# Kernel optimization log

Hardware: AMD Instinct MI355X
Metric: run time of the kernel (lower is better)

The kernel has to match this reference:

```python
import jax, jax.numpy as jnp
import numpy as np

NUM_LAYERS = 16
ALPHA = 1.0
EPS = 1e-20

def setup_inputs() -> dict:
    key = jax.random.key(0)
    k1, k2, k3, k4 = jax.random.split(key, 4)
    B, S, M, G = 8, 9, 8, 512
    M2 = M * M
    return {
        "dict_real": jax.random.normal(k1, (B, S, M2, G), dtype=jnp.float32),
        "dict_imag": jax.random.normal(k2, (B, S, M2, G), dtype=jnp.float32),
        "cov_real": jax.random.normal(k3, (B, S, M, M), dtype=jnp.float32),
        "cov_imag": jax.random.normal(k4, (B, S, M, M), dtype=jnp.float32),
    }

def reference(dict_real, dict_imag, cov_real, cov_imag):
    D = (dict_real + 1j * dict_imag).astype(jnp.complex64)   # (B,S,M2,G) dictionary_band
    C = (cov_real + 1j * cov_imag).astype(jnp.complex64)     # (B,S,M,M) covariance matrix
    B, S, M, _ = C.shape
    G = D.shape[-1]
    # covariance_vector = cov.transpose(2,3).reshape(B,S,M2,1)
    r = jnp.swapaxes(C, 2, 3).reshape(B, S, M * M, 1)
    Dh = jnp.conj(jnp.swapaxes(D, 2, 3))                     # (B,S,G,M2)
    DhD = jnp.matmul(Dh, D)                                  # (B,S,G,G) Hermitian PSD
    Dhr = jnp.matmul(Dh, r)                                  # (B,S,G,1)
    # initial spectrum: real part, L2-normalized over grid dim
    res = jnp.real(Dhr).astype(jnp.float32)
    res = res / (jnp.linalg.norm(res, axis=2, keepdims=True) + EPS)
    # gamma = 1 / max|eig(D^H D)|; Hermitian PSD so eigvalsh gives same max magnitude
    eig = jnp.linalg.eigvalsh(DhD)                           # (B,S,G) real
    gamma = 1.0 / jnp.max(jnp.abs(eig), axis=2, keepdims=True)        # (B,S,1)
    lam = 0.5 * jnp.max(jnp.abs(Dhr), axis=2, keepdims=True).reshape(B, S, 1)
    theta = (ALPHA * lam * gamma).reshape(B, S, 1, 1)
    g = gamma.reshape(B, S, 1, 1).astype(jnp.complex64)
    I = jnp.eye(G, dtype=jnp.complex64)
    Wt = I - g * DhD                                         # (B,S,G,G)
    Wer = g * Dhr                                            # We @ r, constant per layer

    def step(res_c, _):
        s = jnp.matmul(Wt, res_c.astype(jnp.complex64)) + Wer
        res_new = jax.nn.relu(jnp.abs(s) - theta)            # soft-shrinkage on magnitude
        return res_new, res_new

    res_final, res_all = jax.lax.scan(step, res, None, length=NUM_LAYERS)
    result_init_all = jnp.moveaxis(res_all, 0, 2)            # (B,S,L,G,1)

    def minmax_norm(x):
        lo = jnp.min(x, axis=2, keepdims=True)
        hi = jnp.max(x, axis=2, keepdims=True)
        return (x - lo) / (hi - lo + EPS)

    result_ave = minmax_norm(jnp.mean(res_final, axis=1, keepdims=True).astype(jnp.float32))
    result = minmax_norm(res_final)
    return (result, result_ave, result_init_all)
```

## Files before the change

### kernel.cpp

```cpp
#include <hip/hip_runtime.h>
#include <math.h>

#define N_SQ   7
#define INV_P  (1.0f / 256.0f)
#define EPS_F  1e-20f
#define PH     72
#define PQ     67

typedef _Float16 h2    __attribute__((ext_vector_type(2)));
typedef _Float16 f16x8 __attribute__((ext_vector_type(8)));
typedef float    f32x4 __attribute__((ext_vector_type(4)));

__device__ inline float cdot2(h2 a, h2 b, float c) {
#if __has_builtin(__builtin_amdgcn_fdot2)
    return __builtin_amdgcn_fdot2(a, b, c, false);
#else
    return c + (float)a.x * (float)b.x + (float)a.y * (float)b.y;
#endif
}
__device__ inline h2 bch2(unsigned int x) { return __builtin_bit_cast(h2, x); }
__device__ inline h2 bch2f(float x)       { return __builtin_bit_cast(h2, x); }
__device__ inline float bcf(h2 x)         { return __builtin_bit_cast(float, x); }


__global__ __launch_bounds__(512, 1) void ista_main_kernel(
    const float* __restrict__ Dre, const float* __restrict__ Dim,
    const float* __restrict__ Cre, const float* __restrict__ Cim,
    float* __restrict__ out, float* __restrict__ ws)
{
    const int bs = blockIdx.x;
    const int t  = threadIdx.x;
    const int wv = t >> 6;
    const int ln = t & 63;
    const int c16 = ln & 15;
    const int qd  = ln >> 4;
    const float* __restrict__ dre = Dre + (size_t)bs * 32768;
    const float* __restrict__ dim = Dim + (size_t)bs * 32768;

    __shared__ __align__(16) float uBuf[9216];
    _Float16* ShRe = (_Float16*)uBuf;
    _Float16* ShIm = (_Float16*)uBuf + 64 * PH;
    float*    Q1   = uBuf + 4608;
    float*    sUp  = uBuf;
    float*    sHu  = uBuf + 1024;
    _Float16* sResH = (_Float16*)(uBuf + 1152);
    __shared__ __align__(16) float s_r[128];
    __shared__ float s_red[16];
    __shared__ float s_scal[8];

    if (t < 64) {
        int i = t >> 3, j = t & 7;
        s_r[2 * t]     = Cre[bs * 64 + j * 8 + i];
        s_r[2 * t + 1] = Cim[bs * 64 + j * 8 + i];
    }
    __syncthreads();

    float dhr_re = 0.f, dhr_im = 0.f;
    h2 dV[64];
    #pragma unroll
    for (int m = 0; m < 64; ++m) {
        float ar = dre[m * 512 + t], ai = dim[m * 512 + t];
        dV[m] = h2{(_Float16)ar, (_Float16)ai};
        float rr = s_r[2 * m], ri = s_r[2 * m + 1];
        dhr_re += ar * rr + ai * ri;
        dhr_im += ar * ri - ai * rr;
    }
    {
        float sv = dhr_re * dhr_re;
        float mv = sqrtf(dhr_re * dhr_re + dhr_im * dhr_im);
        for (int off = 32; off; off >>= 1) {
            sv += __shfl_down(sv, off, 64);
            mv = fmaxf(mv, __shfl_down(mv, off, 64));
        }
        if (ln == 0) { s_red[wv] = sv; s_red[8 + wv] = mv; }
        __syncthreads();
        if (t == 0) {
            float ss = 0.f, mm = 0.f;
            for (int k = 0; k < 8; ++k) { ss += s_red[k]; mm = fmaxf(mm, s_red[8 + k]); }
            s_scal[7] = ss; s_scal[2] = mm;
        }
        __syncthreads();
    }
    float res_g = dhr_re / (sqrtf(s_scal[7]) + EPS_F);

    const int tau0 = 2 * wv, tau1 = 2 * wv + 1;
    const int I0 = tau0 >> 2, J0 = tau0 & 3;
    const int I1 = tau1 >> 2, J1 = tau1 & 3;

    auto epilogue = [&](f32x4 P0, f32x4 Qa0, f32x4 P1, f32x4 Qa1, bool first, bool last) {
        #pragma unroll
        for (int r = 0; r < 4; ++r) {
            Q1[(I0 * 16 + qd * 4 + r) * PQ + J0 * 16 + c16] = Qa0[r];
            Q1[(I1 * 16 + qd * 4 + r) * PQ + J1 * 16 + c16] = Qa1[r];
        }
        float dv = 0.f;
        if (I0 == J0) {
            #pragma unroll
            for (int r = 0; r < 4; ++r) if (qd * 4 + r == c16) dv = fmaxf(dv, fabsf(P0[r]));
        }
        if (I1 == J1) {
            #pragma unroll
            for (int r = 0; r < 4; ++r) if (qd * 4 + r == c16) dv = fmaxf(dv, fabsf(P1[r]));
        }
        for (int off = 32; off; off >>= 1) dv = fmaxf(dv, __shfl_down(dv, off, 64));
        if (ln == 0) s_red[wv] = dv;
        __syncthreads();
        if (t == 0) {
            float m = 0.f;
            for (int k = 0; k < 8; ++k) m = fmaxf(m, s_red[k]);
            s_scal[3] = first ? logf(m) : 2.f * s_scal[3] + logf(m);
            s_scal[4] = 1.f / m;
        }
        __syncthreads();
        float ic = s_scal[4];
        float ci0[4], ci1[4];
        #pragma unroll
        for (int r = 0; r < 4; ++r) {
            ci0[r] = Qa0[r] - Q1[(J0 * 16 + c16) * PQ + I0 * 16 + qd * 4 + r];
            ci1[r] = Qa1[r] - Q1[(J1 * 16 + c16) * PQ + I1 * 16 + qd * 4 + r];
        }
        if (!last) {
            #pragma unroll
            for (int r = 0; r < 4; ++r) {
                ShRe[(I0 * 16 + qd * 4 + r) * PH + J0 * 16 + c16] = (_Float16)(P0[r] * ic);
                ShIm[(I0 * 16 + qd * 4 + r) * PH + J0 * 16 + c16] = (_Float16)(ci0[r] * ic);
                ShRe[(I1 * 16 + qd * 4 + r) * PH + J1 * 16 + c16] = (_Float16)(P1[r] * ic);
                ShIm[(I1 * 16 + qd * 4 + r) * PH + J1 * 16 + c16] = (_Float16)(ci1[r] * ic);
            }
            __syncthreads();
        } else {
            float fr = 0.f;
            #pragma unroll
            for (int r = 0; r < 4; ++r)
                fr += P0[r] * P0[r] + ci0[r] * ci0[r] + P1[r] * P1[r] + ci1[r] * ci1[r];
            fr *= ic * ic;
            for (int off = 32; off; off >>= 1) fr += __shfl_down(fr, off, 64);
            if (ln == 0) s_red[wv] = fr;
            __syncthreads();
            if (t == 0) {
                float fsum = 0.f;
                for (int k = 0; k < 8; ++k) fsum += s_red[k];
                float loglam = (2.f * s_scal[3] + logf(fsum)) * INV_P;
                float gamma = expf(-loglam);
                s_scal[0] = gamma;
                s_scal[1] = 0.5f * s_scal[2] * gamma;
            }
            __syncthreads();
        }
    };

    h2 du_re[32], du_im[32];
    f32x4 gP0 = {0.f, 0.f, 0.f, 0.f}, gQ0 = {0.f, 0.f, 0.f, 0.f};
    f32x4 gP1 = {0.f, 0.f, 0.f, 0.f}, gQ1 = {0.f, 0.f, 0.f, 0.f};
    {
        const int srow = t >> 4;
        const int scb  = (t & 15) * 4;
        float4 pr0, pi0, pr1, pi1;
        pr0 = *(const float4*)&dre[srow * 512 + scb];
        pi0 = *(const float4*)&dim[srow * 512 + scb];
        pr1 = *(const float4*)&dre[(srow + 32) * 512 + scb];
        pi1 = *(const float4*)&dim[(srow + 32) * 512 + scb];
        for (int ch = 0; ch < 8; ++ch) {
            *(h2*)&ShRe[srow * PH + scb]     = h2{(_Float16)pr0.x, (_Float16)pr0.y};
            *(h2*)&ShRe[srow * PH + scb + 2] = h2{(_Float16)pr0.z, (_Float16)pr0.w};
            *(h2*)&ShIm[srow * PH + scb]     = h2{(_Float16)pi0.x, (_Float16)pi0.y};
            *(h2*)&ShIm[srow * PH + scb + 2] = h2{(_Float16)pi0.z, (_Float16)pi0.w};
            *(h2*)&ShRe[(srow + 32) * PH + scb]     = h2{(_Float16)pr1.x, (_Float16)pr1.y};
            *(h2*)&ShRe[(srow + 32) * PH + scb + 2] = h2{(_Float16)pr1.z, (_Float16)pr1.w};
            *(h2*)&ShIm[(srow + 32) * PH + scb]     = h2{(_Float16)pi1.x, (_Float16)pi1.y};
            *(h2*)&ShIm[(srow + 32) * PH + scb + 2] = h2{(_Float16)pi1.z, (_Float16)pi1.w};
            if (ch < 7) {
                int gc = (ch + 1) * 64;
                pr0 = *(const float4*)&dre[srow * 512 + gc + scb];
                pi0 = *(const float4*)&dim[srow * 512 + gc + scb];
                pr1 = *(const float4*)&dre[(srow + 32) * 512 + gc + scb];
                pi1 = *(const float4*)&dim[(srow + 32) * 512 + gc + scb];
            }
            __syncthreads();
            #pragma unroll
            for (int ks = 0; ks < 64; ks += 32) {
                f16x8 arI0 = *(const f16x8*)&ShRe[(I0 * 16 + c16) * PH + ks + qd * 8];
                f16x8 aiI0 = *(const f16x8*)&ShIm[(I0 * 16 + c16) * PH + ks + qd * 8];
                f16x8 arJ0 = *(const f16x8*)&ShRe[(J0 * 16 + c16) * PH + ks + qd * 8];
                f16x8 aiJ0 = *(const f16x8*)&ShIm[(J0 * 16 + c16) * PH + ks + qd * 8];
                gP0 = __builtin_amdgcn_mfma_f32_16x16x32_f16(arI0, arJ0, gP0, 0, 0, 0);
                gP0 = __builtin_amdgcn_mfma_f32_16x16x32_f16(aiI0, aiJ0, gP0, 0, 0, 0);
                gQ0 = __builtin_amdgcn_mfma_f32_16x16x32_f16(aiI0, arJ0, gQ0, 0, 0, 0);
                f16x8 arI1 = *(const f16x8*)&ShRe[(I1 * 16 + c16) * PH + ks + qd * 8];
                f16x8 aiI1 = *(const f16x8*)&ShIm[(I1 * 16 + c16) * PH + ks + qd * 8];
                f16x8 arJ1 = *(const f16x8*)&ShRe[(J1 * 16 + c16) * PH + ks + qd * 8];
                f16x8 aiJ1 = *(const f16x8*)&ShIm[(J1 * 16 + c16) * PH + ks + qd * 8];
                gP1 = __builtin_amdgcn_mfma_f32_16x16x32_f16(arI1, arJ1, gP1, 0, 0, 0);
                gP1 = __builtin_amdgcn_mfma_f32_16x16x32_f16(aiI1, aiJ1, gP1, 0, 0, 0);
                gQ1 = __builtin_amdgcn_mfma_f32_16x16x32_f16(aiI1, arJ1, gQ1, 0, 0, 0);
            }
            if (ch == wv) {
                #pragma unroll
                for (int c = 0; c < 8; ++c) {
                    uint4 aw = *(const uint4*)&ShRe[ln * PH + 8 * c];
                    du_re[4 * c + 0] = bch2(aw.x); du_re[4 * c + 1] = bch2(aw.y);
                    du_re[4 * c + 2] = bch2(aw.z); du_re[4 * c + 3] = bch2(aw.w);
                    uint4 bw = *(const uint4*)&ShIm[ln * PH + 8 * c];
                    du_im[4 * c + 0] = bch2(bw.x); du_im[4 * c + 1] = bch2(bw.y);
                    du_im[4 * c + 2] = bch2(bw.z); du_im[4 * c + 3] = bch2(bw.w);
                }
            }
            __syncthreads();
        }
    }
    epilogue(gP0, gQ0, gP1, gQ1, true, false);

    for (int sq = 0; sq < N_SQ; ++sq) {
        f32x4 P0 = {0.f, 0.f, 0.f, 0.f}, Qa0 = {0.f, 0.f, 0.f, 0.f};
        f32x4 P1 = {0.f, 0.f, 0.f, 0.f}, Qa1 = {0.f, 0.f, 0.f, 0.f};
        #pragma unroll
        for (int ks = 0; ks < 64; ks += 32) {
            f16x8 arI0 = *(const f16x8*)&ShRe[(I0 * 16 + c16) * PH + ks + qd * 8];
            f16x8 aiI0 = *(const f16x8*)&ShIm[(I0 * 16 + c16) * PH + ks + qd * 8];
            f16x8 arJ0 = *(const f16x8*)&ShRe[(J0 * 16 + c16) * PH + ks + qd * 8];
            f16x8 aiJ0 = *(const f16x8*)&ShIm[(J0 * 16 + c16) * PH + ks + qd * 8];
            P0  = __builtin_amdgcn_mfma_f32_16x16x32_f16(arI0, arJ0, P0, 0, 0, 0);
            P0  = __builtin_amdgcn_mfma_f32_16x16x32_f16(aiI0, aiJ0, P0, 0, 0, 0);
            Qa0 = __builtin_amdgcn_mfma_f32_16x16x32_f16(aiI0, arJ0, Qa0, 0, 0, 0);
            f16x8 arI1 = *(const f16x8*)&ShRe[(I1 * 16 + c16) * PH + ks + qd * 8];
            f16x8 aiI1 = *(const f16x8*)&ShIm[(I1 * 16 + c16) * PH + ks + qd * 8];
            f16x8 arJ1 = *(const f16x8*)&ShRe[(J1 * 16 + c16) * PH + ks + qd * 8];
            f16x8 aiJ1 = *(const f16x8*)&ShIm[(J1 * 16 + c16) * PH + ks + qd * 8];
            P1  = __builtin_amdgcn_mfma_f32_16x16x32_f16(arI1, arJ1, P1, 0, 0, 0);
            P1  = __builtin_amdgcn_mfma_f32_16x16x32_f16(aiI1, aiJ1, P1, 0, 0, 0);
            Qa1 = __builtin_amdgcn_mfma_f32_16x16x32_f16(aiI1, arJ1, Qa1, 0, 0, 0);
        }
        epilogue(P0, Qa0, P1, Qa1, false, sq == N_SQ - 1);
    }

    const float gamma = s_scal[0];
    const float theta = s_scal[1];
    float* out_init = out + 40960 + (size_t)bs * 8192;
    const int resh_base = 64 * wv;

    for (int l = 0; l < 16; ++l) {
        sResH[t] = (_Float16)res_g;
        float upR = 0.f, upI = 0.f;
        #pragma unroll
        for (int c = 0; c < 8; ++c) {
            uint4 rw = *(const uint4*)&sResH[resh_base + 8 * c];
            h2 r0 = bch2(rw.x), r1 = bch2(rw.y), r2 = bch2(rw.z), r3 = bch2(rw.w);
            upR = cdot2(du_re[4 * c + 0], r0, upR);  upI = cdot2(du_im[4 * c + 0], r0, upI);
            upR = cdot2(du_re[4 * c + 1], r1, upR);  upI = cdot2(du_im[4 * c + 1], r1, upI);
            upR = cdot2(du_re[4 * c + 2], r2, upR);  upI = cdot2(du_im[4 * c + 2], r2, upI);
            upR = cdot2(du_re[4 * c + 3], r3, upR);  upI = cdot2(du_im[4 * c + 3], r3, upI);
        }
        *(float2*)&sUp[(wv * 64 + ln) * 2] = make_float2(upR, upI);
        __syncthreads();
        if (wv == 0) {
            float ufR = 0.f, ufI = 0.f;
            #pragma unroll
            for (int w8 = 0; w8 < 8; ++w8) {
                float2 p = *(const float2*)&sUp[(w8 * 64 + ln) * 2];
                ufR += p.x; ufI += p.y;
            }
            h2 hu1 = h2{(_Float16)ufR, (_Float16)ufI};
            h2 hu2 = h2{(_Float16)ufI, (_Float16)(-ufR)};
            *(float2*)&sHu[2 * ln] = make_float2(bcf(hu1), bcf(hu2));
        }
        __syncthreads();
        float wR = 0.f, wI = 0.f;
        #pragma unroll
        for (int mm = 0; mm < 32; ++mm) {
            float4 hq = *(const float4*)&sHu[4 * mm];
            wR = cdot2(dV[2 * mm],     bch2f(hq.x), wR);
            wI = cdot2(dV[2 * mm],     bch2f(hq.y), wI);
            wR = cdot2(dV[2 * mm + 1], bch2f(hq.z), wR);
            wI = cdot2(dV[2 * mm + 1], bch2f(hq.w), wI);
        }
        float sre = res_g + gamma * (dhr_re - wR);
        float sim = gamma * (dhr_im - wI);
        float mag = sqrtf(sre * sre + sim * sim);
        res_g = fmaxf(mag - theta, 0.f);
        out_init[l * 512 + t] = res_g;
    }

    {
        float mn = res_g, mx = res_g;
        for (int off = 32; off; off >>= 1) {
            mn = fminf(mn, __shfl_down(mn, off, 64));
            mx = fmaxf(mx, __shfl_down(mx, off, 64));
        }
        if (ln == 0) { s_red[wv] = mn; s_red[8 + wv] = mx; }
        __syncthreads();
        if (t == 0) {
            float a = s_red[0], b2 = s_red[8];
            for (int k = 1; k < 8; ++k) { a = fminf(a, s_red[k]); b2 = fmaxf(b2, s_red[8 + k]); }
            s_scal[5] = a; s_scal[6] = b2;
        }
        __syncthreads();
        out[bs * 512 + t] = (res_g - s_scal[5]) / (s_scal[6] - s_scal[5] + EPS_F);
        ws[bs * 512 + t] = res_g;
    }
}

__global__ __launch_bounds__(512) void ista_ave_kernel(
    const float* __restrict__ ws, float* __restrict__ out)
{
    const int b = blockIdx.x;
    const int g = threadIdx.x;
    __shared__ float s_red[16];
    __shared__ float s_scal[2];
    float acc = 0.f;
    #pragma unroll
    for (int s = 0; s < 9; ++s) acc += ws[(b * 9 + s) * 512 + g];
    acc *= (1.f / 9.f);
    float mn = acc, mx = acc;
    for (int off = 32; off; off >>= 1) {
        mn = fminf(mn, __shfl_down(mn, off, 64));
        mx = fmaxf(mx, __shfl_down(mx, off, 64));
    }
    if ((g & 63) == 0) { s_red[g >> 6] = mn; s_red[8 + (g >> 6)] = mx; }
    __syncthreads();
    if (g == 0) {
        float a = s_red[0], b2 = s_red[8];
        for (int k = 1; k < 8; ++k) { a = fminf(a, s_red[k]); b2 = fmaxf(b2, s_red[8 + k]); }
        s_scal[0] = a; s_scal[1] = b2;
    }
    __syncthreads();
    out[36864 + b * 512 + g] = (acc - s_scal[0]) / (s_scal[1] - s_scal[0] + EPS_F);
}

extern "C" void kernel_launch(void* const* d_in, const int* in_sizes, int n_in,
                              void* d_out, int out_size, void* d_ws, size_t ws_size,
                              hipStream_t stream) {
    const float* Dre = (const float*)d_in[0];
    const float* Dim = (const float*)d_in[1];
    const float* Cre = (const float*)d_in[2];
    const float* Cim = (const float*)d_in[3];
    float* out = (float*)d_out;
    float* ws  = (float*)d_ws;

    ista_main_kernel<<<72, 512, 0, stream>>>(Dre, Dim, Cre, Cim, out, ws);
    ista_ave_kernel<<<8, 512, 0, stream>>>(ws, out);
}
```

Before: 112.6 us.

## Drop register-resident fp16 dictionary; re-read fp32 D from global each layer

Removes the 64-element per-thread fp16 dictionary cache (dV) and the packed fp16 u vector, and instead re-reads the fp32 dictionary columns from global memory in every layer's D·u product, computed in fp32. The reduction of partial u sums is also spread across all eight waves (eight lanes each) instead of being done by wave 0 alone. The launch bound no longer pins one block per CU. This cuts register pressure and fp16 rounding, at the cost of 16 extra passes over 256 KB of D per block, which should mostly hit cache.

```diff
diff --git a/kernel.cpp b/kernel.cpp
--- a/kernel.cpp
+++ b/kernel.cpp
@@ -19,11 +19,9 @@
 #endif
 }
 __device__ inline h2 bch2(unsigned int x) { return __builtin_bit_cast(h2, x); }
-__device__ inline h2 bch2f(float x)       { return __builtin_bit_cast(h2, x); }
-__device__ inline float bcf(h2 x)         { return __builtin_bit_cast(float, x); }
-
-
-__global__ __launch_bounds__(512, 1) void ista_main_kernel(
+
+
+__global__ __launch_bounds__(512) void ista_main_kernel(
     const float* __restrict__ Dre, const float* __restrict__ Dim,
     const float* __restrict__ Cre, const float* __restrict__ Cim,
     float* __restrict__ out, float* __restrict__ ws)
@@ -56,11 +54,9 @@
     __syncthreads();
 
     float dhr_re = 0.f, dhr_im = 0.f;
-    h2 dV[64];
-    #pragma unroll
+    #pragma unroll 8
     for (int m = 0; m < 64; ++m) {
         float ar = dre[m * 512 + t], ai = dim[m * 512 + t];
-        dV[m] = h2{(_Float16)ar, (_Float16)ai};
         float rr = s_r[2 * m], ri = s_r[2 * m + 1];
         dhr_re += ar * rr + ai * ri;
         dhr_im += ar * ri - ai * rr;
@@ -252,26 +248,24 @@
         }
         *(float2*)&sUp[(wv * 64 + ln) * 2] = make_float2(upR, upI);
         __syncthreads();
-        if (wv == 0) {
+        if (ln < 8) {
+            int m = 8 * wv + ln;
             float ufR = 0.f, ufI = 0.f;
             #pragma unroll
-            for (int w8 = 0; w8 < 8; ++w8) {
-                float2 p = *(const float2*)&sUp[(w8 * 64 + ln) * 2];
-                ufR += p.x; ufI += p.y;
-            }
-            h2 hu1 = h2{(_Float16)ufR, (_Float16)ufI};
-            h2 hu2 = h2{(_Float16)ufI, (_Float16)(-ufR)};
-            *(float2*)&sHu[2 * ln] = make_float2(bcf(hu1), bcf(hu2));
+            for (int p = 0; p < 8; ++p) {
+                float2 q = *(const float2*)&sUp[(p * 64 + m) * 2];
+                ufR += q.x; ufI += q.y;
+            }
+            *(float2*)&sHu[2 * m] = make_float2(ufR, ufI);
         }
         __syncthreads();
         float wR = 0.f, wI = 0.f;
-        #pragma unroll
-        for (int mm = 0; mm < 32; ++mm) {
-            float4 hq = *(const float4*)&sHu[4 * mm];
-            wR = cdot2(dV[2 * mm],     bch2f(hq.x), wR);
-            wI = cdot2(dV[2 * mm],     bch2f(hq.y), wI);
-            wR = cdot2(dV[2 * mm + 1], bch2f(hq.z), wR);
-            wI = cdot2(dV[2 * mm + 1], bch2f(hq.w), wI);
+        #pragma unroll 16
+        for (int m = 0; m < 64; ++m) {
+            float2 uu = *(const float2*)&sHu[2 * m];
+            float ar = dre[m * 512 + t], ai = dim[m * 512 + t];
+            wR += ar * uu.x + ai * uu.y;
+            wI += ar * uu.y - ai * uu.x;
         }
         float sre = res_g + gamma * (dhr_re - wR);
         float sim = gamma * (dhr_im - wI);
```

Result: slower. 149.7 us (+32.9%).

## Use 1024-thread blocks and fuse batch-average via last-block atomic counter

Applied to the files above, without the earlier changes.

Doubles threads per block so each wave computes one 16x16 Gram tile instead of two, and splits the per-grid-point dot products over two half-blocks with a shared-memory reduction. It also removes the separate averaging kernel: each block bumps a per-batch atomic counter and the last of the nine blocks computes the mean and min-max normalisation. This aims to shorten the serial per-block chain and drop one kernel launch. In exchange it adds a memset launch, extra barriers and reductions per layer, and a 1024-thread register budget that may cause spills.

```diff
diff --git a/kernel.cpp b/kernel.cpp
--- a/kernel.cpp
+++ b/kernel.cpp
@@ -23,12 +23,13 @@
 __device__ inline float bcf(h2 x)         { return __builtin_bit_cast(float, x); }
 
 
-__global__ __launch_bounds__(512, 1) void ista_main_kernel(
+__global__ __launch_bounds__(1024) void ista_fused_kernel(
     const float* __restrict__ Dre, const float* __restrict__ Dim,
     const float* __restrict__ Cre, const float* __restrict__ Cim,
-    float* __restrict__ out, float* __restrict__ ws)
+    float* __restrict__ out, float* __restrict__ ws, int* __restrict__ cnt)
 {
     const int bs = blockIdx.x;
+    const int bb = bs / 9;
     const int t  = threadIdx.x;
     const int wv = t >> 6;
     const int ln = t & 63;
@@ -41,12 +42,15 @@
     _Float16* ShRe = (_Float16*)uBuf;
     _Float16* ShIm = (_Float16*)uBuf + 64 * PH;
     float*    Q1   = uBuf + 4608;
+    float*    sDh  = uBuf;
     float*    sUp  = uBuf;
-    float*    sHu  = uBuf + 1024;
-    _Float16* sResH = (_Float16*)(uBuf + 1152);
+    float*    sHu  = uBuf + 2048;
+    _Float16* sResH = (_Float16*)(uBuf + 2176);
+    float*    sW   = uBuf + 2432;
     __shared__ __align__(16) float s_r[128];
-    __shared__ float s_red[16];
+    __shared__ float s_red[32];
     __shared__ float s_scal[8];
+    __shared__ int   sFlag;
 
     if (t < 64) {
         int i = t >> 3, j = t & 7;
@@ -55,91 +59,88 @@
     }
     __syncthreads();
 
+    const int g5 = t & 511;
+    const int mh = t >> 9;
+    h2 dV[32];
     float dhr_re = 0.f, dhr_im = 0.f;
-    h2 dV[64];
-    #pragma unroll
-    for (int m = 0; m < 64; ++m) {
-        float ar = dre[m * 512 + t], ai = dim[m * 512 + t];
-        dV[m] = h2{(_Float16)ar, (_Float16)ai};
-        float rr = s_r[2 * m], ri = s_r[2 * m + 1];
-        dhr_re += ar * rr + ai * ri;
-        dhr_im += ar * ri - ai * rr;
-    }
     {
+        const int mb = mh << 5;
+        #pragma unroll
+        for (int k = 0; k < 32; ++k) {
+            int m = mb + k;
+            float ar = dre[m * 512 + g5], ai = dim[m * 512 + g5];
+            dV[k] = h2{(_Float16)ar, (_Float16)ai};
+            float rr = s_r[2 * m], ri = s_r[2 * m + 1];
+            dhr_re += ar * rr + ai * ri;
+            dhr_im += ar * ri - ai * rr;
+        }
+    }
+    sDh[2 * t] = dhr_re; sDh[2 * t + 1] = dhr_im;
+    __syncthreads();
+    if (t < 512) {
+        dhr_re = sDh[2 * t] + sDh[2 * (t + 512)];
+        dhr_im = sDh[2 * t + 1] + sDh[2 * (t + 512) + 1];
         float sv = dhr_re * dhr_re;
         float mv = sqrtf(dhr_re * dhr_re + dhr_im * dhr_im);
         for (int off = 32; off; off >>= 1) {
             sv += __shfl_down(sv, off, 64);
             mv = fmaxf(mv, __shfl_down(mv, off, 64));
         }
-        if (ln == 0) { s_red[wv] = sv; s_red[8 + wv] = mv; }
-        __syncthreads();
-        if (t == 0) {
-            float ss = 0.f, mm = 0.f;
-            for (int k = 0; k < 8; ++k) { ss += s_red[k]; mm = fmaxf(mm, s_red[8 + k]); }
-            s_scal[7] = ss; s_scal[2] = mm;
-        }
-        __syncthreads();
-    }
-    float res_g = dhr_re / (sqrtf(s_scal[7]) + EPS_F);
-
-    const int tau0 = 2 * wv, tau1 = 2 * wv + 1;
-    const int I0 = tau0 >> 2, J0 = tau0 & 3;
-    const int I1 = tau1 >> 2, J1 = tau1 & 3;
-
-    auto epilogue = [&](f32x4 P0, f32x4 Qa0, f32x4 P1, f32x4 Qa1, bool first, bool last) {
-        #pragma unroll
-        for (int r = 0; r < 4; ++r) {
-            Q1[(I0 * 16 + qd * 4 + r) * PQ + J0 * 16 + c16] = Qa0[r];
-            Q1[(I1 * 16 + qd * 4 + r) * PQ + J1 * 16 + c16] = Qa1[r];
-        }
+        if (ln == 0) { s_red[wv] = sv; s_red[16 + wv] = mv; }
+    }
+    __syncthreads();
+    if (t == 0) {
+        float ss = 0.f, mm = 0.f;
+        for (int k = 0; k < 8; ++k) { ss += s_red[k]; mm = fmaxf(mm, s_red[16 + k]); }
+        s_scal[7] = ss; s_scal[2] = mm;
+    }
+    __syncthreads();
+    float res_g = (t < 512) ? dhr_re / (sqrtf(s_scal[7]) + EPS_F) : 0.f;
+
+    const int I = wv >> 2, J = wv & 3;
+
+    auto epilogue = [&](f32x4 P, f32x4 Qa, bool first, bool last) {
+        #pragma unroll
+        for (int r = 0; r < 4; ++r)
+            Q1[(I * 16 + qd * 4 + r) * PQ + J * 16 + c16] = Qa[r];
         float dv = 0.f;
-        if (I0 == J0) {
-            #pragma unroll
-            for (int r = 0; r < 4; ++r) if (qd * 4 + r == c16) dv = fmaxf(dv, fabsf(P0[r]));
-        }
-        if (I1 == J1) {
-            #pragma unroll
-            for (int r = 0; r < 4; ++r) if (qd * 4 + r == c16) dv = fmaxf(dv, fabsf(P1[r]));
+        if (I == J) {
+            #pragma unroll
+            for (int r = 0; r < 4; ++r) if (qd * 4 + r == c16) dv = fmaxf(dv, fabsf(P[r]));
         }
         for (int off = 32; off; off >>= 1) dv = fmaxf(dv, __shfl_down(dv, off, 64));
         if (ln == 0) s_red[wv] = dv;
         __syncthreads();
         if (t == 0) {
             float m = 0.f;
-            for (int k = 0; k < 8; ++k) m = fmaxf(m, s_red[k]);
+            for (int k = 0; k < 16; ++k) m = fmaxf(m, s_red[k]);
             s_scal[3] = first ? logf(m) : 2.f * s_scal[3] + logf(m);
             s_scal[4] = 1.f / m;
         }
         __syncthreads();
         float ic = s_scal[4];
-        float ci0[4], ci1[4];
-        #pragma unroll
-        for (int r = 0; r < 4; ++r) {
-            ci0[r] = Qa0[r] - Q1[(J0 * 16 + c16) * PQ + I0 * 16 + qd * 4 + r];
-            ci1[r] = Qa1[r] - Q1[(J1 * 16 + c16) * PQ + I1 * 16 + qd * 4 + r];
-        }
+        float ci[4];
+        #pragma unroll
+        for (int r = 0; r < 4; ++r)
+            ci[r] = Qa[r] - Q1[(J * 16 + c16) * PQ + I * 16 + qd * 4 + r];
         if (!last) {
             #pragma unroll
             for (int r = 0; r < 4; ++r) {
-                ShRe[(I0 * 16 + qd * 4 + r) * PH + J0 * 16 + c16] = (_Float16)(P0[r] * ic);
-                ShIm[(I0 * 16 + qd * 4 + r) * PH + J0 * 16 + c16] = (_Float16)(ci0[r] * ic);
-                ShRe[(I1 * 16 + qd * 4 + r) * PH + J1 * 16 + c16] = (_Float16)(P1[r] * ic);
-                ShIm[(I1 * 16 + qd * 4 + r) * PH + J1 * 16 + c16] = (_Float16)(ci1[r] * ic);
+                ShRe[(I * 16 + qd * 4 + r) * PH + J * 16 + c16] = (_Float16)(P[r] * ic);
+                ShIm[(I * 16 + qd * 4 + r) * PH + J * 16 + c16] = (_Float16)(ci[r] * ic);
             }
             __syncthreads();
         } else {
             float fr = 0.f;
             #pragma unroll
-            for (int r = 0; r < 4; ++r)
-                fr += P0[r] * P0[r] + ci0[r] * ci0[r] + P1[r] * P1[r] + ci1[r] * ci1[r];
+            for (int r = 0; r < 4; ++r) fr += P[r] * P[r] + ci[r] * ci[r];
             fr *= ic * ic;
             for (int off = 32; off; off >>= 1) fr += __shfl_down(fr, off, 64);
             if (ln == 0) s_red[wv] = fr;
             __syncthreads();
             if (t == 0) {
                 float fsum = 0.f;
-                for (int k = 0; k < 8; ++k) fsum += s_red[k];
+                for (int k = 0; k < 16; ++k) fsum += s_red[k];
                 float loglam = (2.f * s_scal[3] + logf(fsum)) * INV_P;
                 float gamma = expf(-loglam);
                 s_scal[0] = gamma;
@@ -149,58 +150,42 @@
         }
     };
 
-    h2 du_re[32], du_im[32];
-    f32x4 gP0 = {0.f, 0.f, 0.f, 0.f}, gQ0 = {0.f, 0.f, 0.f, 0.f};
-    f32x4 gP1 = {0.f, 0.f, 0.f, 0.f}, gQ1 = {0.f, 0.f, 0.f, 0.f};
+    h2 du_re[16], du_im[16];
+    f32x4 gP = {0.f, 0.f, 0.f, 0.f}, gQ = {0.f, 0.f, 0.f, 0.f};
     {
         const int srow = t >> 4;
         const int scb  = (t & 15) * 4;
-        float4 pr0, pi0, pr1, pi1;
-        pr0 = *(const float4*)&dre[srow * 512 + scb];
-        pi0 = *(const float4*)&dim[srow * 512 + scb];
-        pr1 = *(const float4*)&dre[(srow + 32) * 512 + scb];
-        pi1 = *(const float4*)&dim[(srow + 32) * 512 + scb];
+        float4 pr0 = *(const float4*)&dre[srow * 512 + scb];
+        float4 pi0 = *(const float4*)&dim[srow * 512 + scb];
+        const int myc = wv >> 1, cb = (wv & 1) * 32;
         for (int ch = 0; ch < 8; ++ch) {
             *(h2*)&ShRe[srow * PH + scb]     = h2{(_Float16)pr0.x, (_Float16)pr0.y};
             *(h2*)&ShRe[srow * PH + scb + 2] = h2{(_Float16)pr0.z, (_Float16)pr0.w};
             *(h2*)&ShIm[srow * PH + scb]     = h2{(_Float16)pi0.x, (_Float16)pi0.y};
             *(h2*)&ShIm[srow * PH + scb + 2] = h2{(_Float16)pi0.z, (_Float16)pi0.w};
-            *(h2*)&ShRe[(srow + 32) * PH + scb]     = h2{(_Float16)pr1.x, (_Float16)pr1.y};
-            *(h2*)&ShRe[(srow + 32) * PH + scb + 2] = h2{(_Float16)pr1.z, (_Float16)pr1.w};
-            *(h2*)&ShIm[(srow + 32) * PH + scb]     = h2{(_Float16)pi1.x, (_Float16)pi1.y};
-            *(h2*)&ShIm[(srow + 32) * PH + scb + 2] = h2{(_Float16)pi1.z, (_Float16)pi1.w};
             if (ch < 7) {
                 int gc = (ch + 1) * 64;
                 pr0 = *(const float4*)&dre[srow * 512 + gc + scb];
                 pi0 = *(const float4*)&dim[srow * 512 + gc + scb];
-                pr1 = *(const float4*)&dre[(srow + 32) * 512 + gc + scb];
-                pi1 = *(const float4*)&dim[(srow + 32) * 512 + gc + scb];
             }
             __syncthreads();
             #pragma unroll
             for (int ks = 0; ks < 64; ks += 32) {
-                f16x8 arI0 = *(const f16x8*)&ShRe[(I0 * 16 + c16) * PH + ks + qd * 8];
-                f16x8 aiI0 = *(const f16x8*)&ShIm[(I0 * 16 + c16) * PH + ks + qd * 8];
-                f16x8 arJ0 = *(const f16x8*)&ShRe[(J0 * 16 + c16) * PH + ks + qd * 8];
-                f16x8 aiJ0 = *(const f16x8*)&ShIm[(J0 * 16 + c16) * PH + ks + qd * 8];
-                gP0 = __builtin_amdgcn_mfma_f32_16x16x32_f16(arI0, arJ0, gP0, 0, 0, 0);
-                gP0 = __builtin_amdgcn_mfma_f32_16x16x32_f16(aiI0, aiJ0, gP0, 0, 0, 0);
-                gQ0 = __builtin_amdgcn_mfma_f32_16x16x32_f16(aiI0, arJ0, gQ0, 0, 0, 0);
-                f16x8 arI1 = *(const f16x8*)&ShRe[(I1 * 16 + c16) * PH + ks + qd * 8];
-                f16x8 aiI1 = *(const f16x8*)&ShIm[(I1 * 16 + c16) * PH + ks + qd * 8];
-                f16x8 arJ1 = *(const f16x8*)&ShRe[(J1 * 16 + c16) * PH + ks + qd * 8];
-                f16x8 aiJ1 = *(const f16x8*)&ShIm[(J1 * 16 + c16) * PH + ks + qd * 8];
-                gP1 = __builtin_amdgcn_mfma_f32_16x16x32_f16(arI1, arJ1, gP1, 0, 0, 0);
-                gP1 = __builtin_amdgcn_mfma_f32_16x16x32_f16(aiI1, aiJ1, gP1, 0, 0, 0);
-                gQ1 = __builtin_amdgcn_mfma_f32_16x16x32_f16(aiI1, arJ1, gQ1, 0, 0, 0);
-            }
-            if (ch == wv) {
+                f16x8 arI = *(const f16x8*)&ShRe[(I * 16 + c16) * PH + ks + qd * 8];
+                f16x8 aiI = *(const f16x8*)&ShIm[(I * 16 + c16) * PH + ks + qd * 8];
+                f16x8 arJ = *(const f16x8*)&ShRe[(J * 16 + c16) * PH + ks + qd * 8];
+                f16x8 aiJ = *(const f16x8*)&ShIm[(J * 16 + c16) * PH + ks + qd * 8];
+                gP = __builtin_amdgcn_mfma_f32_16x16x32_f16(arI, arJ, gP, 0, 0, 0);
+                gP = __builtin_amdgcn_mfma_f32_16x16x32_f16(aiI, aiJ, gP, 0, 0, 0);
+                gQ = __builtin_amdgcn_mfma_f32_16x16x32_f16(aiI, arJ, gQ, 0, 0, 0);
+            }
+            if (ch == myc) {
                 #pragma unroll
-                for (int c = 0; c < 8; ++c) {
-                    uint4 aw = *(const uint4*)&ShRe[ln * PH + 8 * c];
+                for (int c = 0; c < 4; ++c) {
+                    uint4 aw = *(const uint4*)&ShRe[ln * PH + cb + 8 * c];
                     du_re[4 * c + 0] = bch2(aw.x); du_re[4 * c + 1] = bch2(aw.y);
                     du_re[4 * c + 2] = bch2(aw.z); du_re[4 * c + 3] = bch2(aw.w);
-                    uint4 bw = *(const uint4*)&ShIm[ln * PH + 8 * c];
+                    uint4 bw = *(const uint4*)&ShIm[ln * PH + cb + 8 * c];
                     du_im[4 * c + 0] = bch2(bw.x); du_im[4 * c + 1] = bch2(bw.y);
                     du_im[4 * c + 2] = bch2(bw.z); du_im[4 * c + 3] = bch2(bw.w);
                 }
@@ -208,41 +193,34 @@
             __syncthreads();
         }
     }
-    epilogue(gP0, gQ0, gP1, gQ1, true, false);
+    epilogue(gP, gQ, true, false);
 
     for (int sq = 0; sq < N_SQ; ++sq) {
-        f32x4 P0 = {0.f, 0.f, 0.f, 0.f}, Qa0 = {0.f, 0.f, 0.f, 0.f};
-        f32x4 P1 = {0.f, 0.f, 0.f, 0.f}, Qa1 = {0.f, 0.f, 0.f, 0.f};
+        f32x4 P = {0.f, 0.f, 0.f, 0.f}, Qa = {0.f, 0.f, 0.f, 0.f};
         #pragma unroll
         for (int ks = 0; ks < 64; ks += 32) {
-            f16x8 arI0 = *(const f16x8*)&ShRe[(I0 * 16 + c16) * PH + ks + qd * 8];
-            f16x8 aiI0 = *(const f16x8*)&ShIm[(I0 * 16 + c16) * PH + ks + qd * 8];
-            f16x8 arJ0 = *(const f16x8*)&ShRe[(J0 * 16 + c16) * PH + ks + qd * 8];
-            f16x8 aiJ0 = *(const f16x8*)&ShIm[(J0 * 16 + c16) * PH + ks + qd * 8];
-            P0  = __builtin_amdgcn_mfma_f32_16x16x32_f16(arI0, arJ0, P0, 0, 0, 0);
-            P0  = __builtin_amdgcn_mfma_f32_16x16x32_f16(aiI0, aiJ0, P0, 0, 0, 0);
-            Qa0 = __builtin_amdgcn_mfma_f32_16x16x32_f16(aiI0, arJ0, Qa0, 0, 0, 0);
-            f16x8 arI1 = *(const f16x8*)&ShRe[(I1 * 16 + c16) * PH + ks + qd * 8];
-            f16x8 aiI1 = *(const f16x8*)&ShIm[(I1 * 16 + c16) * PH + ks + qd * 8];
-            f16x8 arJ1 = *(const f16x8*)&ShRe[(J1 * 16 + c16) * PH + ks + qd * 8];
-            f16x8 aiJ1 = *(const f16x8*)&ShIm[(J1 * 16 + c16) * PH + ks + qd * 8];
-            P1  = __builtin_amdgcn_mfma_f32_16x16x32_f16(arI1, arJ1, P1, 0, 0, 0);
-            P1  = __builtin_amdgcn_mfma_f32_16x16x32_f16(aiI1, aiJ1, P1, 0, 0, 0);
-            Qa1 = __builtin_amdgcn_mfma_f32_16x16x32_f16(aiI1, arJ1, Qa1, 0, 0, 0);
-        }
-        epilogue(P0, Qa0, P1, Qa1, false, sq == N_SQ - 1);
+            f16x8 arI = *(const f16x8*)&ShRe[(I * 16 + c16) * PH + ks + qd * 8];
+            f16x8 aiI = *(const f16x8*)&ShIm[(I * 16 + c16) * PH + ks + qd * 8];
+            f16x8 arJ = *(const f16x8*)&ShRe[(J * 16 + c16) * PH + ks + qd * 8];
+            f16x8 aiJ = *(const f16x8*)&ShIm[(J * 16 + c16) * PH + ks + qd * 8];
+            P  = __builtin_amdgcn_mfma_f32_16x16x32_f16(arI, arJ, P, 0, 0, 0);
+            P  = __builtin_amdgcn_mfma_f32_16x16x32_f16(aiI, aiJ, P, 0, 0, 0);
+            Qa = __builtin_amdgcn_mfma_f32_16x16x32_f16(aiI, arJ, Qa, 0, 0, 0);
+        }
+        epilogue(P, Qa, false, sq == N_SQ - 1);
     }
 
     const float gamma = s_scal[0];
     const float theta = s_scal[1];
     float* out_init = out + 40960 + (size_t)bs * 8192;
-    const int resh_base = 64 * wv;
+    const int resh_base = 32 * wv;
 
     for (int l = 0; l < 16; ++l) {
-        sResH[t] = (_Float16)res_g;
+        if (t < 512) sResH[t] = (_Float16)res_g;
+        __syncthreads();
         float upR = 0.f, upI = 0.f;
         #pragma unroll
-        for (int c = 0; c < 8; ++c) {
+        for (int c = 0; c < 4; ++c) {
             uint4 rw = *(const uint4*)&sResH[resh_base + 8 * c];
             h2 r0 = bch2(rw.x), r1 = bch2(rw.y), r2 = bch2(rw.z), r3 = bch2(rw.w);
             upR = cdot2(du_re[4 * c + 0], r0, upR);  upI = cdot2(du_im[4 * c + 0], r0, upI);
@@ -250,80 +228,96 @@
             upR = cdot2(du_re[4 * c + 2], r2, upR);  upI = cdot2(du_im[4 * c + 2], r2, upI);
             upR = cdot2(du_re[4 * c + 3], r3, upR);  upI = cdot2(du_im[4 * c + 3], r3, upI);
         }
-        *(float2*)&sUp[(wv * 64 + ln) * 2] = make_float2(upR, upI);
-        __syncthreads();
-        if (wv == 0) {
+        *(float2*)&sUp[wv * 128 + 2 * ln] = make_float2(upR, upI);
+        __syncthreads();
+        if (t < 64) {
             float ufR = 0.f, ufI = 0.f;
             #pragma unroll
-            for (int w8 = 0; w8 < 8; ++w8) {
-                float2 p = *(const float2*)&sUp[(w8 * 64 + ln) * 2];
-                ufR += p.x; ufI += p.y;
+            for (int p = 0; p < 16; ++p) {
+                float2 q = *(const float2*)&sUp[p * 128 + 2 * t];
+                ufR += q.x; ufI += q.y;
             }
             h2 hu1 = h2{(_Float16)ufR, (_Float16)ufI};
             h2 hu2 = h2{(_Float16)ufI, (_Float16)(-ufR)};
-            *(float2*)&sHu[2 * ln] = make_float2(bcf(hu1), bcf(hu2));
+            *(float2*)&sHu[2 * t] = make_float2(bcf(hu1), bcf(hu2));
         }
         __syncthreads();
         float wR = 0.f, wI = 0.f;
-        #pragma unroll
-        for (int mm = 0; mm < 32; ++mm) {
-            float4 hq = *(const float4*)&sHu[4 * mm];
-            wR = cdot2(dV[2 * mm],     bch2f(hq.x), wR);
-            wI = cdot2(dV[2 * mm],     bch2f(hq.y), wI);
-            wR = cdot2(dV[2 * mm + 1], bch2f(hq.z), wR);
-            wI = cdot2(dV[2 * mm + 1], bch2f(hq.w), wI);
-        }
-        float sre = res_g + gamma * (dhr_re - wR);
-        float sim = gamma * (dhr_im - wI);
-        float mag = sqrtf(sre * sre + sim * sim);
-        res_g = fmaxf(mag - theta, 0.f);
-        out_init[l * 512 + t] = res_g;
-    }
-
-    {
+        {
+            const int pb = 16 * mh;
+            #pragma unroll
+            for (int j = 0; j < 16; ++j) {
+                float4 hq = *(const float4*)&sHu[4 * (pb + j)];
+                wR = cdot2(dV[2 * j],     bch2f(hq.x), wR);
+                wI = cdot2(dV[2 * j],     bch2f(hq.y), wI);
+                wR = cdot2(dV[2 * j + 1], bch2f(hq.z), wR);
+                wI = cdot2(dV[2 * j + 1], bch2f(hq.w), wI);
+            }
+        }
+        *(float2*)&sW[mh * 1024 + 2 * g5] = make_float2(wR, wI);
+        __syncthreads();
+        if (t < 512) {
+            float2 wa = *(const float2*)&sW[2 * t];
+            float2 wb = *(const float2*)&sW[1024 + 2 * t];
+            float sre = res_g + gamma * (dhr_re - (wa.x + wb.x));
+            float sim = gamma * (dhr_im - (wa.y + wb.y));
+            float mag = sqrtf(sre * sre + sim * sim);
+            res_g = fmaxf(mag - theta, 0.f);
+            out_init[l * 512 + t] = res_g;
+        }
+    }
+
+    if (t < 512) {
         float mn = res_g, mx = res_g;
         for (int off = 32; off; off >>= 1) {
             mn = fminf(mn, __shfl_down(mn, off, 64));
             mx = fmaxf(mx, __shfl_down(mx, off, 64));
         }
-        if (ln == 0) { s_red[wv] = mn; s_red[8 + wv] = mx; }
-        __syncthreads();
-        if (t == 0) {
-            float a = s_red[0], b2 = s_red[8];
-            for (int k = 1; k < 8; ++k) { a = fminf(a, s_red[k]); b2 = fmaxf(b2, s_red[8 + k]); }
-            s_scal[5] = a; s_scal[6] = b2;
-        }
-        __syncthreads();
+        if (ln == 0) { s_red[wv] = mn; s_red[16 + wv] = mx; }
+    }
+    __syncthreads();
+    if (t == 0) {
+        float a = s_red[0], b2 = s_red[16];
+        for (int k = 1; k < 8; ++k) { a = fminf(a, s_red[k]); b2 = fmaxf(b2, s_red[16 + k]); }
+        s_scal[5] = a; s_scal[6] = b2;
+    }
+    __syncthreads();
+    if (t < 512) {
         out[bs * 512 + t] = (res_g - s_scal[5]) / (s_scal[6] - s_scal[5] + EPS_F);
         ws[bs * 512 + t] = res_g;
     }
-}
-
-__global__ __launch_bounds__(512) void ista_ave_kernel(
-    const float* __restrict__ ws, float* __restrict__ out)
-{
-    const int b = blockIdx.x;
-    const int g = threadIdx.x;
-    __shared__ float s_red[16];
-    __shared__ float s_scal[2];
-    float acc = 0.f;
-    #pragma unroll
-    for (int s = 0; s < 9; ++s) acc += ws[(b * 9 + s) * 512 + g];
-    acc *= (1.f / 9.f);
-    float mn = acc, mx = acc;
-    for (int off = 32; off; off >>= 1) {
-        mn = fminf(mn, __shfl_down(mn, off, 64));
-        mx = fmaxf(mx, __shfl_down(mx, off, 64));
-    }
-    if ((g & 63) == 0) { s_red[g >> 6] = mn; s_red[8 + (g >> 6)] = mx; }
-    __syncthreads();
-    if (g == 0) {
-        float a = s_red[0], b2 = s_red[8];
-        for (int k = 1; k < 8; ++k) { a = fminf(a, s_red[k]); b2 = fmaxf(b2, s_red[8 + k]); }
-        s_scal[0] = a; s_scal[1] = b2;
-    }
-    __syncthreads();
-    out[36864 + b * 512 + g] = (acc - s_scal[0]) / (s_scal[1] - s_scal[0] + EPS_F);
+    __threadfence();
+    __syncthreads();
+
+    if (t == 0) {
+        int old = __hip_atomic_fetch_add(&cnt[bb], 1, __ATOMIC_ACQ_REL, __HIP_MEMORY_SCOPE_AGENT);
+        sFlag = (old == 8) ? 1 : 0;
+    }
+    __syncthreads();
+    if (sFlag) {
+        __threadfence();
+        float acc = 0.f;
+        if (t < 512) {
+            #pragma unroll
+            for (int s = 0; s < 9; ++s) acc += ws[(bb * 9 + s) * 512 + t];
+            acc *= (1.f / 9.f);
+            float mn = acc, mx = acc;
+            for (int off = 32; off; off >>= 1) {
+                mn = fminf(mn, __shfl_down(mn, off, 64));
+                mx = fmaxf(mx, __shfl_down(mx, off, 64));
+            }
+            if (ln == 0) { s_red[wv] = mn; s_red[16 + wv] = mx; }
+        }
+        __syncthreads();
+        if (t == 0) {
+            float a = s_red[0], b2 = s_red[16];
+            for (int k = 1; k < 8; ++k) { a = fminf(a, s_red[k]); b2 = fmaxf(b2, s_red[16 + k]); }
+            s_scal[5] = a; s_scal[6] = b2;
+        }
+        __syncthreads();
+        if (t < 512)
+            out[36864 + bb * 512 + t] = (acc - s_scal[5]) / (s_scal[6] - s_scal[5] + EPS_F);
+    }
 }
 
 extern "C" void kernel_launch(void* const* d_in, const int* in_sizes, int n_in,
@@ -335,7 +329,8 @@
     const float* Cim = (const float*)d_in[3];
     float* out = (float*)d_out;
     float* ws  = (float*)d_ws;
-
-    ista_main_kernel<<<72, 512, 0, stream>>>(Dre, Dim, Cre, Cim, out, ws);
-    ista_ave_kernel<<<8, 512, 0, stream>>>(ws, out);
+    int*   cnt = (int*)((char*)d_ws + 147456);
+
+    hipMemsetAsync(cnt, 0, 8 * sizeof(int), stream);
+    ista_fused_kernel<<<72, 1024, 0, stream>>>(Dre, Dim, Cre, Cim, out, ws, cnt);
 }
```

Result: slower. 157.9 us (+40.2%).
